# Optimization experiments

Measured on AMD Instinct MI355X. Metric: run time of the kernel, lower is better.

## Reference

```python
import jax, jax.numpy as jnp
import numpy as np

NUM_NT = 1024
DIM = 64
B, N = 64, 4096


def setup_inputs() -> dict:
    key = jax.random.key(0)
    k1, k2 = jax.random.split(key)
    codes = jax.random.normal(k1, (B, N, DIM), dtype=jnp.float32)
    cb = jax.random.normal(k2, (NUM_NT, DIM), dtype=jnp.float32)
    # VanillaCodebook init: F.normalize -> L2-normalize each row
    codebook = cb / jnp.maximum(jnp.linalg.norm(cb, axis=-1, keepdims=True), 1e-12)
    return {"codes": codes, "codebook": codebook}


def reference(codes, codebook):
    x_sq = jnp.sum(codes * codes, axis=-1, keepdims=True)          # (B, N, 1)
    c_sq = jnp.sum(codebook * codebook, axis=-1)                   # (NT,)
    xc = jnp.einsum('bnd,kd->bnk', codes, codebook)                # (B, N, NT)
    dist2 = x_sq - 2.0 * xc + c_sq                                 # (B, N, NT)
    quant_id = jnp.argmin(dist2, axis=-1)                          # (B, N)
    quant_codes = codebook[quant_id]                               # (B, N, D)
    return quant_codes, quant_id
```

## Files before the change

kernel.cpp:

```cpp
#include <hip/hip_runtime.h>


#define NUM_NT 1024
#define DIM 64
#define M_TOTAL (64 * 4096)
#define NTILES 64
#define THR 1.0e-3f

typedef __attribute__((ext_vector_type(8))) short short8;
typedef __attribute__((ext_vector_type(4))) float f32x4;

static __device__ __forceinline__ unsigned short f2bf_rne(float f) {
    unsigned u = __builtin_bit_cast(unsigned, f);
    u += 0x7FFFu + ((u >> 16) & 1u);
    return (unsigned short)(u >> 16);
}
static __device__ __forceinline__ float bf2f(unsigned short h) {
    unsigned u = ((unsigned)h) << 16;
    return __builtin_bit_cast(float, u);
}

__global__ __launch_bounds__(64) void csq_kernel(const float* __restrict__ cb,
                                                 float* __restrict__ hcsq,
                                                 int* __restrict__ counter) {
    int k = blockIdx.x, d = threadIdx.x;
    if (k == 0 && d == 0) *counter = 0;
    float v = cb[k * DIM + d];
    float s = v * v;
    #pragma unroll
    for (int off = 32; off > 0; off >>= 1) s += __shfl_down(s, off);
    if (d == 0) hcsq[k] = 0.5f * s;
}

__global__ __launch_bounds__(256) void cb_convert(const float* __restrict__ cb,
                                                  short8* __restrict__ bh,
                                                  short8* __restrict__ bl) {
    int gtid = blockIdx.x * 256 + threadIdx.x;
    int f = gtid >> 6;
    int lane = gtid & 63;
    int t = f >> 1, kk = f & 1;
    int n = t * 16 + (lane & 15);
    int k0 = kk * 32 + 8 * (lane >> 4);
    const float* p = cb + n * DIM + k0;
    short8 h, l;
    #pragma unroll
    for (int e = 0; e < 8; ++e) {
        float v = p[e];
        unsigned short hb = f2bf_rne(v);
        h[e] = (short)hb;
        l[e] = (short)f2bf_rne(v - bf2f(hb));
    }
    bh[f * 64 + lane] = h;
    bl[f * 64 + lane] = l;
}

__global__ __launch_bounds__(256, 2) void vq_approx(const float* __restrict__ codes,
                                                    const short8* __restrict__ bh,
                                                    const short8* __restrict__ bl,
                                                    const float* __restrict__ hcsq,
                                                    float* __restrict__ out_ids,
                                                    int* __restrict__ worklist,
                                                    int* __restrict__ counter) {
    const int lane = threadIdx.x & 63;
    const int wv   = threadIdx.x >> 6;
    const int qb   = (blockIdx.x * 4 + wv) * 64;
    const int c16  = lane & 15;
    const int kg   = lane >> 4;

    short8 ah[4][2], al[4][2];
    #pragma unroll
    for (int s = 0; s < 4; ++s) {
        const float* xr = codes + (size_t)(qb + s * 16 + c16) * DIM + kg * 8;
        #pragma unroll
        for (int e = 0; e < 8; ++e) {
            float v = -xr[e];
            unsigned short hb = f2bf_rne(v);
            ah[s][0][e] = (short)hb;
            al[s][0][e] = (short)f2bf_rne(v - bf2f(hb));
            float w = -xr[32 + e];
            unsigned short hw = f2bf_rne(w);
            ah[s][1][e] = (short)hw;
            al[s][1][e] = (short)f2bf_rne(w - bf2f(hw));
        }
    }

    float d1[16], d2[16];
    int   tb[16];
    #pragma unroll
    for (int r = 0; r < 16; ++r) { d1[r] = 3.4e38f; d2[r] = 3.4e38f; tb[r] = 0; }

    short8 pvh0 = bh[0 * 64 + lane];
    short8 pvl0 = bl[0 * 64 + lane];
    short8 pvh1 = bh[1 * 64 + lane];
    short8 pvl1 = bl[1 * 64 + lane];
    float  phc  = hcsq[c16];

    for (int t = 0; t < NTILES; ++t) {
        short8 vh0 = pvh0, vl0 = pvl0, vh1 = pvh1, vl1 = pvl1;
        float  hc  = phc;
        if (t + 1 < NTILES) {
            pvh0 = bh[(t * 2 + 2) * 64 + lane];
            pvl0 = bl[(t * 2 + 2) * 64 + lane];
            pvh1 = bh[(t * 2 + 3) * 64 + lane];
            pvl1 = bl[(t * 2 + 3) * 64 + lane];
            phc  = hcsq[(t + 1) * 16 + c16];
        }
        f32x4 hcv = {hc, hc, hc, hc};
        #pragma unroll
        for (int s = 0; s < 4; ++s) {
            f32x4 acc = hcv;
            acc = __builtin_amdgcn_mfma_f32_16x16x32_bf16(ah[s][0], vh0, acc, 0, 0, 0);
            acc = __builtin_amdgcn_mfma_f32_16x16x32_bf16(al[s][0], vh0, acc, 0, 0, 0);
            acc = __builtin_amdgcn_mfma_f32_16x16x32_bf16(ah[s][0], vl0, acc, 0, 0, 0);
            acc = __builtin_amdgcn_mfma_f32_16x16x32_bf16(ah[s][1], vh1, acc, 0, 0, 0);
            acc = __builtin_amdgcn_mfma_f32_16x16x32_bf16(al[s][1], vh1, acc, 0, 0, 0);
            acc = __builtin_amdgcn_mfma_f32_16x16x32_bf16(ah[s][1], vl1, acc, 0, 0, 0);
            #pragma unroll
            for (int rr = 0; rr < 4; ++rr) {
                float d = acc[rr];
                int r = s * 4 + rr;
                bool take = d < d1[r];
                d2[r] = __builtin_amdgcn_fmed3f(d1[r], d2[r], d);
                d1[r] = fminf(d1[r], d);
                tb[r] = take ? t : tb[r];
            }
        }
    }

    #pragma unroll
    for (int r = 0; r < 16; ++r) {
        float dd1 = d1[r], dd2 = d2[r];
        int idv = tb[r] * 16 + c16;
        #pragma unroll
        for (int m = 1; m < 16; m <<= 1) {
            float d_o  = __shfl_xor(dd1, m, 64);
            int   i_o  = __shfl_xor(idv, m, 64);
            float d2_o = __shfl_xor(dd2, m, 64);
            float nd2 = fminf(fminf(dd2, d2_o), fmaxf(dd1, d_o));
            bool take = (d_o < dd1) || (d_o == dd1 && i_o < idv);
            dd1 = take ? d_o : dd1;
            idv = take ? i_o : idv;
            dd2 = nd2;
        }
        if (c16 == 0) {
            int q = qb + (r >> 2) * 16 + kg * 4 + (r & 3);
            out_ids[q] = (float)idv;
            if (dd2 - dd1 < THR) {
                int slot = atomicAdd(counter, 1);
                worklist[slot] = q;
            }
        }
    }
}

__global__ __launch_bounds__(256) void vq_fixup(const float* __restrict__ codes,
                                                const float* __restrict__ cb,
                                                const float* __restrict__ hcsq,
                                                const int* __restrict__ worklist,
                                                const int* __restrict__ counter,
                                                float* __restrict__ out_ids) {
    const int lane = threadIdx.x & 63;
    const int wid  = blockIdx.x * 4 + (threadIdx.x >> 6);
    const int nw   = gridDim.x * 4;
    const int cnt  = *counter;

    for (int w = wid; w < cnt; w += nw) {
        const int q = worklist[w];
        float x[64];
        const float4* xp = reinterpret_cast<const float4*>(codes + (size_t)q * DIM);
        #pragma unroll
        for (int i = 0; i < 16; ++i) {
            float4 v = xp[i];
            x[4*i+0] = v.x; x[4*i+1] = v.y; x[4*i+2] = v.z; x[4*i+3] = v.w;
        }
        float best = 3.4e38f; int bid = 0;
        for (int jj = 0; jj < 16; ++jj) {
            int k = jj * 64 + lane;
            const float4* cp = reinterpret_cast<const float4*>(cb + (size_t)k * DIM);
            float acc = hcsq[k];
            #pragma unroll
            for (int i = 0; i < 16; ++i) {
                float4 c = cp[i];
                acc = fmaf(-x[4*i+0], c.x, acc);
                acc = fmaf(-x[4*i+1], c.y, acc);
                acc = fmaf(-x[4*i+2], c.z, acc);
                acc = fmaf(-x[4*i+3], c.w, acc);
            }
            if (acc < best) { best = acc; bid = k; }
        }
        #pragma unroll
        for (int m = 1; m < 64; m <<= 1) {
            float d_o = __shfl_xor(best, m, 64);
            int   i_o = __shfl_xor(bid, m, 64);
            bool take = (d_o < best) || (d_o == best && i_o < bid);
            best = take ? d_o : best;
            bid  = take ? i_o : bid;
        }
        int id = __shfl(bid, 0, 64);
        if (lane == 0) out_ids[q] = (float)id;
    }
}

__global__ __launch_bounds__(256) void vq_gather(const float* __restrict__ cb,
                                                 const float* __restrict__ out_ids,
                                                 float4* __restrict__ out_codes4) {
    const int base = blockIdx.x * 256 + threadIdx.x;
    const int STRIDE = 4096 * 256;
    const float4* cb4 = reinterpret_cast<const float4*>(cb);

    float fids[4];
    #pragma unroll
    for (int u = 0; u < 4; ++u)
        fids[u] = out_ids[(base + u * STRIDE) >> 4];

    #pragma unroll
    for (int u = 0; u < 4; ++u) {
        int i = base + u * STRIDE;
        int id = (int)fids[u];
        out_codes4[i] = cb4[id * 16 + (i & 15)];
    }
}

extern "C" void kernel_launch(void* const* d_in, const int* in_sizes, int n_in,
                              void* d_out, int out_size, void* d_ws, size_t ws_size,
                              hipStream_t stream) {
    const float* codes = (const float*)d_in[0];
    const float* cb    = (const float*)d_in[1];
    float* out         = (float*)d_out;

    float* out_codes = out;
    float* out_ids   = out + (size_t)M_TOTAL * DIM;

    float*  hcsq     = (float*)d_ws;
    short8* bh       = (short8*)((char*)d_ws + 4096);
    short8* bl       = (short8*)((char*)d_ws + 4096 + 128 * 1024);
    int*    counter  = (int*)((char*)d_ws + 264 * 1024);
    int*    worklist = (int*)((char*)d_ws + 268 * 1024);

    csq_kernel<<<NUM_NT, 64, 0, stream>>>(cb, hcsq, counter);
    cb_convert<<<32, 256, 0, stream>>>(cb, bh, bl);
    vq_approx<<<M_TOTAL / 256, 256, 0, stream>>>(codes, bh, bl, hcsq,
                                                 out_ids, worklist, counter);
    vq_fixup<<<512, 256, 0, stream>>>(codes, cb, hcsq, worklist, counter, out_ids);
    vq_gather<<<4096, 256, 0, stream>>>(cb, out_ids, (float4*)out_codes);
}
```

Measured before the change: 160.6 us.

## Stage codebook tiles in shared memory and halve queries per wave

Each wave now handles 32 queries instead of 64, and the grid is doubled to match. Codebook hi/lo bf16 fragments are loaded cooperatively into a double-buffered LDS tile, one quarter per wave, instead of every wave fetching all fragments from global memory. This cuts global/L2 traffic and register pressure so more waves can be resident. In exchange it adds a block-wide barrier on every tile iteration and halves the MFMA work done per codebook fragment load.

```diff
diff --git a/kernel.cpp b/kernel.cpp
--- a/kernel.cpp
+++ b/kernel.cpp
@@ -54,22 +54,28 @@
     bl[f * 64 + lane] = l;
 }
 
-__global__ __launch_bounds__(256, 2) void vq_approx(const float* __restrict__ codes,
-                                                    const short8* __restrict__ bh,
-                                                    const short8* __restrict__ bl,
-                                                    const float* __restrict__ hcsq,
-                                                    float* __restrict__ out_ids,
-                                                    int* __restrict__ worklist,
-                                                    int* __restrict__ counter) {
-    const int lane = threadIdx.x & 63;
-    const int wv   = threadIdx.x >> 6;
-    const int qb   = (blockIdx.x * 4 + wv) * 64;
+__global__ __launch_bounds__(256) void vq_approx(const float* __restrict__ codes,
+                                                 const short8* __restrict__ bh,
+                                                 const short8* __restrict__ bl,
+                                                 const float* __restrict__ hcsq,
+                                                 float* __restrict__ out_ids,
+                                                 int* __restrict__ worklist,
+                                                 int* __restrict__ counter) {
+    __shared__ short8 lb[2][2][2][64];
+    const int tid  = threadIdx.x;
+    const int lane = tid & 63;
+    const int wv   = tid >> 6;
+    const int qb   = (blockIdx.x * 4 + wv) * 32;
     const int c16  = lane & 15;
     const int kg   = lane >> 4;
 
-    short8 ah[4][2], al[4][2];
-    #pragma unroll
-    for (int s = 0; s < 4; ++s) {
+    const int sarr = (tid >> 7) & 1;
+    const int skk  = (tid >> 6) & 1;
+    const short8* __restrict__ sptr = sarr ? bl : bh;
+
+    short8 ah[2][2], al[2][2];
+    #pragma unroll
+    for (int s = 0; s < 2; ++s) {
         const float* xr = codes + (size_t)(qb + s * 16 + c16) * DIM + kg * 8;
         #pragma unroll
         for (int e = 0; e < 8; ++e) {
@@ -84,30 +90,28 @@
         }
     }
 
-    float d1[16], d2[16];
-    int   tb[16];
-    #pragma unroll
-    for (int r = 0; r < 16; ++r) { d1[r] = 3.4e38f; d2[r] = 3.4e38f; tb[r] = 0; }
-
-    short8 pvh0 = bh[0 * 64 + lane];
-    short8 pvl0 = bl[0 * 64 + lane];
-    short8 pvh1 = bh[1 * 64 + lane];
-    short8 pvl1 = bl[1 * 64 + lane];
-    float  phc  = hcsq[c16];
+    float d1[8], d2[8];
+    int   tb[8];
+    #pragma unroll
+    for (int r = 0; r < 8; ++r) { d1[r] = 3.4e38f; d2[r] = 3.4e38f; tb[r] = 0; }
+
+    lb[0][sarr][skk][lane] = sptr[(0 * 2 + skk) * 64 + lane];
+    __syncthreads();
 
     for (int t = 0; t < NTILES; ++t) {
-        short8 vh0 = pvh0, vl0 = pvl0, vh1 = pvh1, vl1 = pvl1;
-        float  hc  = phc;
-        if (t + 1 < NTILES) {
-            pvh0 = bh[(t * 2 + 2) * 64 + lane];
-            pvl0 = bl[(t * 2 + 2) * 64 + lane];
-            pvh1 = bh[(t * 2 + 3) * 64 + lane];
-            pvl1 = bl[(t * 2 + 3) * 64 + lane];
-            phc  = hcsq[(t + 1) * 16 + c16];
-        }
+        const int cur = t & 1;
+        short8 stg;
+        if (t + 1 < NTILES)
+            stg = sptr[((t + 1) * 2 + skk) * 64 + lane];
+
+        short8 vh0 = lb[cur][0][0][lane];
+        short8 vh1 = lb[cur][0][1][lane];
+        short8 vl0 = lb[cur][1][0][lane];
+        short8 vl1 = lb[cur][1][1][lane];
+        float hc = hcsq[t * 16 + c16];
         f32x4 hcv = {hc, hc, hc, hc};
         #pragma unroll
-        for (int s = 0; s < 4; ++s) {
+        for (int s = 0; s < 2; ++s) {
             f32x4 acc = hcv;
             acc = __builtin_amdgcn_mfma_f32_16x16x32_bf16(ah[s][0], vh0, acc, 0, 0, 0);
             acc = __builtin_amdgcn_mfma_f32_16x16x32_bf16(al[s][0], vh0, acc, 0, 0, 0);
@@ -125,10 +129,14 @@
                 tb[r] = take ? t : tb[r];
             }
         }
-    }
-
-    #pragma unroll
-    for (int r = 0; r < 16; ++r) {
+
+        if (t + 1 < NTILES)
+            lb[cur ^ 1][sarr][skk][lane] = stg;
+        __syncthreads();
+    }
+
+    #pragma unroll
+    for (int r = 0; r < 8; ++r) {
         float dd1 = d1[r], dd2 = d2[r];
         int idv = tb[r] * 16 + c16;
         #pragma unroll
@@ -239,7 +247,7 @@
 
     csq_kernel<<<NUM_NT, 64, 0, stream>>>(cb, hcsq, counter);
     cb_convert<<<32, 256, 0, stream>>>(cb, bh, bl);
-    vq_approx<<<M_TOTAL / 256, 256, 0, stream>>>(codes, bh, bl, hcsq,
+    vq_approx<<<M_TOTAL / 128, 256, 0, stream>>>(codes, bh, bl, hcsq,
                                                  out_ids, worklist, counter);
     vq_fixup<<<512, 256, 0, stream>>>(codes, cb, hcsq, worklist, counter, out_ids);
     vq_gather<<<4096, 256, 0, stream>>>(cb, out_ids, (float4*)out_codes);
```

Measured after the change: 171.9 us. 1.07x slower.
